# Kernel optimization log

Hardware: AMD Instinct MI355X
Metric: run time of the kernel (lower is better)

The kernel has to match this reference:

```python
import jax, jax.numpy as jnp
from jax import lax
import numpy as np

B, W, F, D = 48, 8192, 64, 128  # batch, input_window, c_in, d_model


def setup_inputs() -> dict:
    key = jax.random.key(0)
    k0, k1, k2, k3 = jax.random.split(key, 4)
    x = jax.random.normal(k0, (B, W, F), jnp.float32)
    # ContextConv(c_in->c_in, k=3): conv1d over time, zero 'same' padding (repo layer, assumed standard conv)
    ctx_w = jax.random.normal(k1, (F, F, 3), jnp.float32) * (2.0 / (F * 3)) ** 0.5
    ctx_b = jnp.zeros((F,), jnp.float32)
    # tokenConv: Conv1d(c_in -> d_model, k=3, circular padding, no bias), kaiming fan_in
    token_w = jax.random.normal(k2, (D, F, 3), jnp.float32) * (2.0 / (F * 3)) ** 0.5
    # seW: Linear(c_in -> input_window)
    seW_w = jax.random.normal(k3, (W, F), jnp.float32) * (1.0 / F) ** 0.5
    seW_b = jnp.zeros((W,), jnp.float32)
    return dict(x=x, ctx_w=ctx_w, ctx_b=ctx_b, token_w=token_w, seW_w=seW_w, seW_b=seW_b)


def _conv1d_ncw(x_ncw, w_oiw, padding):
    return lax.conv_general_dilated(
        x_ncw, w_oiw, window_strides=(1,), padding=padding,
        dimension_numbers=("NCW", "OIW", "NCW"))


def reference(x, ctx_w, ctx_b, token_w, seW_w, seW_b):
    # ---- contextConv: (B,W,F) -> (B,W,F), conv over time ----
    xc = _conv1d_ncw(x.transpose(0, 2, 1), ctx_w, [(1, 1)])  # (B,F,W)
    xc = (xc + ctx_b[None, :, None]).transpose(0, 2, 1)       # (B,W,F)

    # ---- structure_embedding (src is detached in torch) ----
    src = lax.stop_gradient(x)
    srcn = src / jnp.linalg.norm(src, axis=-1, keepdims=True)         # row-normalize each timestep
    gram = jnp.einsum('bwf,bwg->bfg', srcn, srcn)                      # batched f x f matmul
    xse = jax.nn.relu(jnp.einsum('bfg,wg->bfw', gram, seW_w) + seW_b[None, None, :])  # (B,F,W)
    xse = xse.transpose(0, 2, 1)                                       # (B,W,F)

    # ---- tokenConv with circular padding ----
    h = (xc + xse).transpose(0, 2, 1)                                  # (B,F,W)
    hp = jnp.pad(h, ((0, 0), (0, 0), (1, 1)), mode='wrap')
    out = _conv1d_ncw(hp, token_w, 'VALID')                            # (B,D,W)
    return out.transpose(0, 2, 1)                                      # (B,W,D)
```

## Files before the change

### kernel.cpp

```cpp
#include <hip/hip_runtime.h>
#include <stdint.h>

#define Bb 48
#define Ww 8192
#define Ff 64
#define Dd 128
#define TWt 64
#define NSLAB 32

#define WS_GRAMP 0u
#define WS_GRAM  25165824u
#define WS_TWT   25952256u
#define WS_CWT   26001408u
#define WS_GBF   26025984u
#define WS_SWB   26419200u
#define WS_RINV  27467776u
#define WS_XBF   29040640u
#define WS_TOTAL (29040640ull + 50331648ull)

typedef __bf16 bf16x8 __attribute__((ext_vector_type(8)));
typedef float f32x4 __attribute__((ext_vector_type(4)));

__device__ __forceinline__ float bf2f(unsigned short u){
  union { unsigned int i; float f; } v; v.i = ((unsigned int)u) << 16; return v.f;
}
__device__ __forceinline__ unsigned short f2bf(float f){
  union { float f; unsigned int i; } v; v.f = f;
  unsigned int i = v.i;
  return (unsigned short)((i + 0x7fffu + ((i >> 16) & 1u)) >> 16);
}
__device__ __forceinline__ f32x4 mfma16(bf16x8 a, bf16x8 b, f32x4 c){
  return __builtin_amdgcn_mfma_f32_16x16x32_bf16(a, b, c, 0, 0, 0);
}

__global__ __launch_bounds__(256) void pack_weights(const float* __restrict__ ctx_w,
                                                    const float* __restrict__ token_w,
                                                    unsigned short* __restrict__ cwT,
                                                    unsigned short* __restrict__ twT)
{
  int idx = blockIdx.x * 256 + threadIdx.x;
  const int ntw = Dd * 192;
  if (idx < ntw){
    int d = idx / 192, kim = idx % 192;
    int ktap = kim >> 6, fi = kim & 63;
    twT[idx] = f2bf(token_w[(d * Ff + fi) * 3 + ktap]);
  } else if (idx < ntw + Ff * 192){
    int i2 = idx - ntw;
    int f = i2 / 192, kim = i2 % 192;
    int ktap = kim >> 6, fi = kim & 63;
    cwT[i2] = f2bf(ctx_w[(f * Ff + fi) * 3 + ktap]);
  }
}

__global__ __launch_bounds__(256) void convert_sew(const float* __restrict__ src,
                                                   unsigned short* __restrict__ dst)
{
  int i = (blockIdx.x * 256 + threadIdx.x) * 8;
  float4 a0 = *(const float4*)(src + i);
  float4 a1 = *(const float4*)(src + i + 4);
  union { uint4 q; unsigned short s[8]; } u;
  u.s[0]=f2bf(a0.x); u.s[1]=f2bf(a0.y); u.s[2]=f2bf(a0.z); u.s[3]=f2bf(a0.w);
  u.s[4]=f2bf(a1.x); u.s[5]=f2bf(a1.y); u.s[6]=f2bf(a1.z); u.s[7]=f2bf(a1.w);
  *(uint4*)(dst + i) = u.q;
}

__global__ __launch_bounds__(256) void xprep(const float* __restrict__ x,
                                             unsigned short* __restrict__ xbf,
                                             float* __restrict__ rinvb)
{
  int tid = blockIdx.x * 256 + threadIdx.x;
  int row = tid >> 2;
  int f0  = (tid & 3) * 16;
  const float* xr = x + (size_t)row * Ff + f0;
  float v[16];
  *(float4*)(v)      = *(const float4*)(xr);
  *(float4*)(v + 4)  = *(const float4*)(xr + 4);
  *(float4*)(v + 8)  = *(const float4*)(xr + 8);
  *(float4*)(v + 12) = *(const float4*)(xr + 12);
  float ss = 0.f;
#pragma unroll
  for (int i = 0; i < 16; ++i) ss += v[i] * v[i];
  ss += __shfl_xor(ss, 1);
  ss += __shfl_xor(ss, 2);
  float rinv = rsqrtf(ss);
  union { uint4 q[2]; unsigned short s[16]; } u;
#pragma unroll
  for (int i = 0; i < 16; ++i) u.s[i] = f2bf(v[i]);
  unsigned short* dst = xbf + (size_t)row * Ff + f0;
  *(uint4*)(dst)     = u.q[0];
  *(uint4*)(dst + 8) = u.q[1];
  if ((tid & 3) == 0) rinvb[row] = rinv;
}

__global__ __launch_bounds__(256) void gram_kernel(const float* __restrict__ x,
                                                   const unsigned short* __restrict__ xbf,
                                                   const float* __restrict__ rinvb,
                                                   float* __restrict__ gramP,
                                                   int fast)
{
  const int b = blockIdx.y;
  const int w_base = blockIdx.x * (Ww / NSLAB);
  const int t = threadIdx.x;
  const int lane = t & 63;
  const int wave = t >> 6;
  const int lrow = lane & 15;
  const int lk = lane >> 4;

  __shared__ unsigned short st[64 * 72];

  f32x4 acc[4] = {};

  const int wl = t >> 2;
  const int f0 = (t & 3) * 16;

  for (int sc = 0; sc < (Ww / NSLAB) / 64; ++sc) {
    const int w0 = w_base + sc * 64;
    const size_t rowg = (size_t)b * Ww + (size_t)(w0 + wl);
    if (fast){
      union { uint4 q; unsigned short s[8]; } a0, a1;
      a0.q = *(const uint4*)(xbf + rowg * Ff + f0);
      a1.q = *(const uint4*)(xbf + rowg * Ff + f0 + 8);
      float rinv = rinvb[rowg];
#pragma unroll
      for (int i = 0; i < 8; ++i) st[(f0 + i) * 72 + wl]     = f2bf(bf2f(a0.s[i]) * rinv);
#pragma unroll
      for (int i = 0; i < 8; ++i) st[(f0 + 8 + i) * 72 + wl] = f2bf(bf2f(a1.s[i]) * rinv);
    } else {
      const float* xr = x + rowg * Ff + f0;
      float v[16];
      *(float4*)(v)      = *(const float4*)(xr);
      *(float4*)(v + 4)  = *(const float4*)(xr + 4);
      *(float4*)(v + 8)  = *(const float4*)(xr + 8);
      *(float4*)(v + 12) = *(const float4*)(xr + 12);
      float ss = 0.f;
#pragma unroll
      for (int i = 0; i < 16; ++i) ss += v[i] * v[i];
      ss += __shfl_xor(ss, 1);
      ss += __shfl_xor(ss, 2);
      float rinv = rsqrtf(ss);
#pragma unroll
      for (int i = 0; i < 16; ++i) st[(f0 + i) * 72 + wl] = f2bf(v[i] * rinv);
    }
    __syncthreads();
#pragma unroll
    for (int kc = 0; kc < 2; ++kc){
      const int kw = kc * 32 + lk * 8;
      bf16x8 bf = *(const bf16x8*)(st + (wave * 16 + lrow) * 72 + kw);
#pragma unroll
      for (int mt = 0; mt < 4; ++mt){
        bf16x8 af = *(const bf16x8*)(st + (mt * 16 + lrow) * 72 + kw);
        acc[mt] = mfma16(af, bf, acc[mt]);
      }
    }
    __syncthreads();
  }

  float* gb = gramP + ((size_t)(blockIdx.x * Bb + b)) * 4096;
#pragma unroll
  for (int mt = 0; mt < 4; ++mt)
#pragma unroll
    for (int r = 0; r < 4; ++r){
      int f = mt * 16 + lk * 4 + r;
      int g = wave * 16 + lrow;
      gb[f * 64 + g] = acc[mt][r];
    }
}

__global__ __launch_bounds__(256) void gram_reduce(const float* __restrict__ gramP,
                                                   float* __restrict__ gram,
                                                   unsigned short* __restrict__ gbf,
                                                   int fast)
{
  int i = blockIdx.x * 256 + threadIdx.x;
  int b = i >> 10;
  int q = i & 1023;
  float sx = 0.f, sy = 0.f, sz = 0.f, sw = 0.f;
#pragma unroll
  for (int sl = 0; sl < NSLAB; ++sl){
    const float4 v = *(const float4*)(gramP + (((size_t)(sl * Bb + b)) << 12) + q * 4);
    sx += v.x; sy += v.y; sz += v.z; sw += v.w;
  }
  float4 s = make_float4(sx, sy, sz, sw);
  *(float4*)(gram + (((size_t)b) << 12) + q * 4) = s;
  if (fast){
    union { unsigned long long u; unsigned short h[4]; } u;
    u.h[0] = f2bf(sx); u.h[1] = f2bf(sy); u.h[2] = f2bf(sz); u.h[3] = f2bf(sw);
    *(unsigned long long*)(gbf + (((size_t)b) << 12) + q * 4) = u.u;
  }
}

#define XSP 72
#define SSP 72
#define HSP 72

__global__ __launch_bounds__(256, 4) void fused_kernel(
    const float* __restrict__ x,
    const unsigned short* __restrict__ xbf,
    const float* __restrict__ ctx_b,
    const float* __restrict__ seW_w,
    const unsigned short* __restrict__ sWb,
    const float* __restrict__ seW_b,
    const float* __restrict__ gram,
    const unsigned short* __restrict__ gbf,
    const unsigned short* __restrict__ cwT,
    const unsigned short* __restrict__ twT,
    float* __restrict__ out,
    int fast)
{
  const int b = blockIdx.y;
  const int w0 = blockIdx.x * TWt;
  const int t = threadIdx.x;
  const int lane = t & 63;
  const int wave = t >> 6;
  const int lrow = lane & 15;
  const int lk = lane >> 4;

  __shared__ __align__(16) unsigned char smem[(84 * XSP + 80 * SSP + 66 * HSP) * 2];
  unsigned short* xs  = (unsigned short*)smem;
  unsigned short* sws = xs + 84 * XSP;
  unsigned short* hsh = sws + 80 * SSP;

  if (fast){
    for (int item = t; item < 84 * 8; item += 256){
      int i = item >> 3, seg = item & 7;
      int c = w0 - 2 + i;
      uint4 val = make_uint4(0u,0u,0u,0u);
      if (c >= 0 && c < Ww) val = *(const uint4*)(xbf + ((size_t)b*Ww + c)*Ff + seg*8);
      *(uint4*)(xs + i*XSP + seg*8) = val;
    }
    for (int item = t; item < 80 * 8; item += 256){
      int i = item >> 3, seg = item & 7;
      int hc = (w0 - 1 + i) & (Ww - 1);
      *(uint4*)(sws + i*SSP + seg*8) = *(const uint4*)(sWb + (size_t)hc*Ff + seg*8);
    }
  } else {
    for (int item = t; item < 84 * 8; item += 256){
      int i = item >> 3, seg = item & 7;
      int c = w0 - 2 + i;
      union { uint4 q; unsigned short s[8]; } u;
      if (c >= 0 && c < Ww){
        const float* xr = x + ((size_t)b*Ww + c)*Ff + seg*8;
        float4 a0 = *(const float4*)(xr);
        float4 a1 = *(const float4*)(xr + 4);
        u.s[0]=f2bf(a0.x); u.s[1]=f2bf(a0.y); u.s[2]=f2bf(a0.z); u.s[3]=f2bf(a0.w);
        u.s[4]=f2bf(a1.x); u.s[5]=f2bf(a1.y); u.s[6]=f2bf(a1.z); u.s[7]=f2bf(a1.w);
      } else {
        u.q = make_uint4(0u,0u,0u,0u);
      }
      *(uint4*)(xs + i*XSP + seg*8) = u.q;
    }
  }
  __syncthreads();

  const int nt = wave;
  bf16x8 cw_frag[6];
  {
    const unsigned short* p = cwT + (nt*16 + lrow)*192 + lk*8;
#pragma unroll
    for (int kc = 0; kc < 6; ++kc) cw_frag[kc] = *(const bf16x8*)(p + kc*32);
  }
  bf16x8 se_frag[2];
  if (fast){
    const unsigned short* gp = gbf + (size_t)b*4096 + (nt*16 + lrow)*64;
#pragma unroll
    for (int kc = 0; kc < 2; ++kc) se_frag[kc] = *(const bf16x8*)(gp + kc*32 + lk*8);
  } else {
    const float* gb = gram + (size_t)b * 4096;
#pragma unroll
    for (int kc = 0; kc < 2; ++kc){
      union { bf16x8 v; unsigned short s[8]; } u;
#pragma unroll
      for (int j = 0; j < 8; ++j){
        int g = kc*32 + lk*8 + j;
        u.s[j] = f2bf(gb[g*64 + nt*16 + lrow]);
      }
      se_frag[kc] = u.v;
    }
  }

  f32x4 xc_acc[5] = {};
  f32x4 se_acc[5] = {};

#pragma unroll
  for (int mt = 0; mt < 5; ++mt){
#pragma unroll
    for (int kc = 0; kc < 6; ++kc){
      int kim = kc*32 + lk*8;
      int ktap = kim >> 6, fi = kim & 63;
      bf16x8 a = *(const bf16x8*)(xs + (mt*16 + lrow + ktap)*XSP + fi);
      xc_acc[mt] = mfma16(a, cw_frag[kc], xc_acc[mt]);
    }
    if (fast){
#pragma unroll
      for (int kc = 0; kc < 2; ++kc){
        bf16x8 a = *(const bf16x8*)(sws + (mt*16 + lrow)*SSP + kc*32 + lk*8);
        se_acc[mt] = mfma16(a, se_frag[kc], se_acc[mt]);
      }
    } else {
      int hc = (w0 - 1 + mt*16 + lrow) & (Ww - 1);
      const float* sp = seW_w + (size_t)hc * Ff;
#pragma unroll
      for (int kc = 0; kc < 2; ++kc){
        union { bf16x8 v; unsigned short s[8]; } u;
        float4 a0 = *(const float4*)(sp + kc*32 + lk*8);
        float4 a1 = *(const float4*)(sp + kc*32 + lk*8 + 4);
        u.s[0]=f2bf(a0.x); u.s[1]=f2bf(a0.y); u.s[2]=f2bf(a0.z); u.s[3]=f2bf(a0.w);
        u.s[4]=f2bf(a1.x); u.s[5]=f2bf(a1.y); u.s[6]=f2bf(a1.z); u.s[7]=f2bf(a1.w);
        se_acc[mt] = mfma16(u.v, se_frag[kc], se_acc[mt]);
      }
    }
  }

  {
    float cb = ctx_b[nt*16 + lrow];
#pragma unroll
    for (int mt = 0; mt < 5; ++mt){
#pragma unroll
      for (int r = 0; r < 4; ++r){
        int j = mt*16 + lk*4 + r;
        if (j < 66){
          int hc = (w0 - 1 + j) & (Ww - 1);
          float se = se_acc[mt][r] + seW_b[hc];
          se = se > 0.f ? se : 0.f;
          hsh[j*HSP + nt*16 + lrow] = f2bf(xc_acc[mt][r] + cb + se);
        }
      }
    }
  }
  __syncthreads();

  if (blockIdx.x == 0 || blockIdx.x == (Ww/TWt - 1)){
    const int j  = (blockIdx.x == 0) ? 0 : 65;
    const int hc = (blockIdx.x == 0) ? (Ww - 1) : 0;
    if (t < 64){
      const int f = t;
      float a = ctx_b[f];
      for (int ktap = 0; ktap < 3; ++ktap){
        int c = hc + ktap - 1;
        if (c >= 0 && c < Ww){
          const float* xr = x + ((size_t)b*Ww + c)*Ff;
          const unsigned short* wr = cwT + f*192 + ktap*64;
          for (int fi = 0; fi < 64; ++fi) a += xr[fi] * bf2f(wr[fi]);
        }
      }
      const float* gb = gram + (size_t)b * 4096;
      const float* sp = seW_w + (size_t)hc * Ff;
      float se = seW_b[hc];
      for (int g = 0; g < 64; ++g) se += sp[g] * gb[g*64 + f];
      se = se > 0.f ? se : 0.f;
      hsh[j*HSP + f] = f2bf(a + se);
    }
    __syncthreads();
  }

  bf16x8 tw_frag[2][6];
#pragma unroll
  for (int q = 0; q < 2; ++q){
    const unsigned short* p = twT + ((wave*2 + q)*16 + lrow)*192 + lk*8;
#pragma unroll
    for (int kc = 0; kc < 6; ++kc) tw_frag[q][kc] = *(const bf16x8*)(p + kc*32);
  }
  f32x4 oacc[4][2] = {};
#pragma unroll
  for (int mt = 0; mt < 4; ++mt){
#pragma unroll
    for (int kc = 0; kc < 6; ++kc){
      int kim = kc*32 + lk*8;
      int ktap = kim >> 6, fi = kim & 63;
      bf16x8 a = *(const bf16x8*)(hsh + (mt*16 + lrow + ktap)*HSP + fi);
#pragma unroll
      for (int q = 0; q < 2; ++q)
        oacc[mt][q] = mfma16(a, tw_frag[q][kc], oacc[mt][q]);
    }
  }

#pragma unroll
  for (int mt = 0; mt < 4; ++mt){
#pragma unroll
    for (int q = 0; q < 2; ++q)
#pragma unroll
      for (int r = 0; r < 4; ++r){
        int row = w0 + mt*16 + lk*4 + r;
        int d   = (wave*2 + q)*16 + lrow;
        out[((size_t)b*Ww + row)*Dd + d] = oacc[mt][q][r];
      }
  }
}

extern "C" void kernel_launch(void* const* d_in, const int* in_sizes, int n_in,
                              void* d_out, int out_size, void* d_ws, size_t ws_size,
                              hipStream_t stream)
{
  const float* x       = (const float*)d_in[0];
  const float* ctx_w   = (const float*)d_in[1];
  const float* ctx_b   = (const float*)d_in[2];
  const float* token_w = (const float*)d_in[3];
  const float* seW_w   = (const float*)d_in[4];
  const float* seW_b   = (const float*)d_in[5];
  float* out = (float*)d_out;

  char* ws = (char*)d_ws;
  float*          gramP = (float*)(ws + WS_GRAMP);
  float*          gram  = (float*)(ws + WS_GRAM);
  unsigned short* twT   = (unsigned short*)(ws + WS_TWT);
  unsigned short* cwT   = (unsigned short*)(ws + WS_CWT);
  unsigned short* gbf   = (unsigned short*)(ws + WS_GBF);
  unsigned short* sWb   = (unsigned short*)(ws + WS_SWB);
  float*          rinvb = (float*)(ws + WS_RINV);
  unsigned short* xbf   = (unsigned short*)(ws + WS_XBF);

  const int fast = (ws_size >= (size_t)WS_TOTAL) ? 1 : 0;

  pack_weights<<<dim3(144), dim3(256), 0, stream>>>(ctx_w, token_w, cwT, twT);
  if (fast){
    convert_sew<<<dim3(256), dim3(256), 0, stream>>>(seW_w, sWb);
    xprep<<<dim3(6144), dim3(256), 0, stream>>>(x, xbf, rinvb);
  }
  gram_kernel<<<dim3(NSLAB, Bb), dim3(256), 0, stream>>>(x, xbf, rinvb, gramP, fast);
  gram_reduce<<<dim3(192), dim3(256), 0, stream>>>(gramP, gram, gbf, fast);
  fused_kernel<<<dim3(Ww/TWt, Bb), dim3(256), 0, stream>>>(
      x, xbf, ctx_b, seW_w, sWb, seW_b, gram, gbf, cwT, twT, out, fast);
}
```

Baseline: 370.8 us.

## Fuse x bf16 conversion into gram kernel, merge weight prep, alias LDS

After: 382.0 us. +3.0%, slower.

```diff
diff --git a/kernel.cpp b/kernel.cpp
--- a/kernel.cpp
+++ b/kernel.cpp
@@ -14,9 +14,8 @@
 #define WS_CWT   26001408u
 #define WS_GBF   26025984u
 #define WS_SWB   26419200u
-#define WS_RINV  27467776u
-#define WS_XBF   29040640u
-#define WS_TOTAL (29040640ull + 50331648ull)
+#define WS_XBF   27467776u
+#define WS_TOTAL (27467776ull + 50331648ull)
 
 typedef __bf16 bf16x8 __attribute__((ext_vector_type(8)));
 typedef float f32x4 __attribute__((ext_vector_type(4)));
@@ -33,70 +32,43 @@
   return __builtin_amdgcn_mfma_f32_16x16x32_bf16(a, b, c, 0, 0, 0);
 }
 
-__global__ __launch_bounds__(256) void pack_weights(const float* __restrict__ ctx_w,
+__global__ __launch_bounds__(256) void prep_weights(const float* __restrict__ ctx_w,
                                                     const float* __restrict__ token_w,
+                                                    const float* __restrict__ seW_w,
                                                     unsigned short* __restrict__ cwT,
-                                                    unsigned short* __restrict__ twT)
+                                                    unsigned short* __restrict__ twT,
+                                                    unsigned short* __restrict__ sWb,
+                                                    int fast)
 {
-  int idx = blockIdx.x * 256 + threadIdx.x;
-  const int ntw = Dd * 192;
-  if (idx < ntw){
-    int d = idx / 192, kim = idx % 192;
-    int ktap = kim >> 6, fi = kim & 63;
-    twT[idx] = f2bf(token_w[(d * Ff + fi) * 3 + ktap]);
-  } else if (idx < ntw + Ff * 192){
-    int i2 = idx - ntw;
-    int f = i2 / 192, kim = i2 % 192;
-    int ktap = kim >> 6, fi = kim & 63;
-    cwT[i2] = f2bf(ctx_w[(f * Ff + fi) * 3 + ktap]);
-  }
-}
-
-__global__ __launch_bounds__(256) void convert_sew(const float* __restrict__ src,
-                                                   unsigned short* __restrict__ dst)
-{
-  int i = (blockIdx.x * 256 + threadIdx.x) * 8;
-  float4 a0 = *(const float4*)(src + i);
-  float4 a1 = *(const float4*)(src + i + 4);
-  union { uint4 q; unsigned short s[8]; } u;
-  u.s[0]=f2bf(a0.x); u.s[1]=f2bf(a0.y); u.s[2]=f2bf(a0.z); u.s[3]=f2bf(a0.w);
-  u.s[4]=f2bf(a1.x); u.s[5]=f2bf(a1.y); u.s[6]=f2bf(a1.z); u.s[7]=f2bf(a1.w);
-  *(uint4*)(dst + i) = u.q;
-}
-
-__global__ __launch_bounds__(256) void xprep(const float* __restrict__ x,
-                                             unsigned short* __restrict__ xbf,
-                                             float* __restrict__ rinvb)
-{
-  int tid = blockIdx.x * 256 + threadIdx.x;
-  int row = tid >> 2;
-  int f0  = (tid & 3) * 16;
-  const float* xr = x + (size_t)row * Ff + f0;
-  float v[16];
-  *(float4*)(v)      = *(const float4*)(xr);
-  *(float4*)(v + 4)  = *(const float4*)(xr + 4);
-  *(float4*)(v + 8)  = *(const float4*)(xr + 8);
-  *(float4*)(v + 12) = *(const float4*)(xr + 12);
-  float ss = 0.f;
-#pragma unroll
-  for (int i = 0; i < 16; ++i) ss += v[i] * v[i];
-  ss += __shfl_xor(ss, 1);
-  ss += __shfl_xor(ss, 2);
-  float rinv = rsqrtf(ss);
-  union { uint4 q[2]; unsigned short s[16]; } u;
-#pragma unroll
-  for (int i = 0; i < 16; ++i) u.s[i] = f2bf(v[i]);
-  unsigned short* dst = xbf + (size_t)row * Ff + f0;
-  *(uint4*)(dst)     = u.q[0];
-  *(uint4*)(dst + 8) = u.q[1];
-  if ((tid & 3) == 0) rinvb[row] = rinv;
+  const int bx = blockIdx.x;
+  if (bx < 144){
+    int idx = bx * 256 + threadIdx.x;
+    const int ntw = Dd * 192;
+    if (idx < ntw){
+      int d = idx / 192, kim = idx % 192;
+      int ktap = kim >> 6, fi = kim & 63;
+      twT[idx] = f2bf(token_w[(d * Ff + fi) * 3 + ktap]);
+    } else if (idx < ntw + Ff * 192){
+      int i2 = idx - ntw;
+      int f = i2 / 192, kim = i2 % 192;
+      int ktap = kim >> 6, fi = kim & 63;
+      cwT[i2] = f2bf(ctx_w[(f * Ff + fi) * 3 + ktap]);
+    }
+  } else if (fast){
+    int i = ((bx - 144) * 256 + threadIdx.x) * 8;
+    float4 a0 = *(const float4*)(seW_w + i);
+    float4 a1 = *(const float4*)(seW_w + i + 4);
+    union { uint4 q; unsigned short s[8]; } u;
+    u.s[0]=f2bf(a0.x); u.s[1]=f2bf(a0.y); u.s[2]=f2bf(a0.z); u.s[3]=f2bf(a0.w);
+    u.s[4]=f2bf(a1.x); u.s[5]=f2bf(a1.y); u.s[6]=f2bf(a1.z); u.s[7]=f2bf(a1.w);
+    *(uint4*)(sWb + i) = u.q;
+  }
 }
 
 __global__ __launch_bounds__(256) void gram_kernel(const float* __restrict__ x,
-                                                   const unsigned short* __restrict__ xbf,
-                                                   const float* __restrict__ rinvb,
+                                                   unsigned short* __restrict__ xbf,
                                                    float* __restrict__ gramP,
-                                                   int fast)
+                                                   int writeXbf)
 {
   const int b = blockIdx.y;
   const int w_base = blockIdx.x * (Ww / NSLAB);
@@ -113,46 +85,63 @@
   const int wl = t >> 2;
   const int f0 = (t & 3) * 16;
 
-  for (int sc = 0; sc < (Ww / NSLAB) / 64; ++sc) {
-    const int w0 = w_base + sc * 64;
-    const size_t rowg = (size_t)b * Ww + (size_t)(w0 + wl);
-    if (fast){
-      union { uint4 q; unsigned short s[8]; } a0, a1;
-      a0.q = *(const uint4*)(xbf + rowg * Ff + f0);
-      a1.q = *(const uint4*)(xbf + rowg * Ff + f0 + 8);
-      float rinv = rinvb[rowg];
-#pragma unroll
-      for (int i = 0; i < 8; ++i) st[(f0 + i) * 72 + wl]     = f2bf(bf2f(a0.s[i]) * rinv);
-#pragma unroll
-      for (int i = 0; i < 8; ++i) st[(f0 + 8 + i) * 72 + wl] = f2bf(bf2f(a1.s[i]) * rinv);
-    } else {
-      const float* xr = x + rowg * Ff + f0;
-      float v[16];
-      *(float4*)(v)      = *(const float4*)(xr);
-      *(float4*)(v + 4)  = *(const float4*)(xr + 4);
-      *(float4*)(v + 8)  = *(const float4*)(xr + 8);
-      *(float4*)(v + 12) = *(const float4*)(xr + 12);
-      float ss = 0.f;
-#pragma unroll
-      for (int i = 0; i < 16; ++i) ss += v[i] * v[i];
-      ss += __shfl_xor(ss, 1);
-      ss += __shfl_xor(ss, 2);
-      float rinv = rsqrtf(ss);
-#pragma unroll
-      for (int i = 0; i < 16; ++i) st[(f0 + i) * 72 + wl] = f2bf(v[i] * rinv);
-    }
+  float v[16];
+  {
+    const float* xr = x + ((size_t)b * Ww + (size_t)(w_base + wl)) * Ff + f0;
+    *(float4*)(v)      = *(const float4*)(xr);
+    *(float4*)(v + 4)  = *(const float4*)(xr + 4);
+    *(float4*)(v + 8)  = *(const float4*)(xr + 8);
+    *(float4*)(v + 12) = *(const float4*)(xr + 12);
+  }
+
+  for (int sc = 0; sc < 4; ++sc) {
+    const size_t rowg = (size_t)b * Ww + (size_t)(w_base + sc * 64 + wl);
+
+    float ss = 0.f;
+#pragma unroll
+    for (int i = 0; i < 16; ++i) ss += v[i] * v[i];
+    ss += __shfl_xor(ss, 1);
+    ss += __shfl_xor(ss, 2);
+    float rinv = rsqrtf(ss);
+
+    union { uint4 q[2]; unsigned short s[16]; } u;
+#pragma unroll
+    for (int i = 0; i < 16; ++i){
+      u.s[i] = f2bf(v[i]);
+      st[(f0 + i) * 72 + wl] = f2bf(v[i] * rinv);
+    }
+    if (writeXbf){
+      unsigned short* dst = xbf + rowg * Ff + f0;
+      *(uint4*)(dst)     = u.q[0];
+      *(uint4*)(dst + 8) = u.q[1];
+    }
+
+    float vn[16];
+    if (sc < 3){
+      const float* xr = x + ((size_t)b * Ww + (size_t)(w_base + (sc+1) * 64 + wl)) * Ff + f0;
+      *(float4*)(vn)      = *(const float4*)(xr);
+      *(float4*)(vn + 4)  = *(const float4*)(xr + 4);
+      *(float4*)(vn + 8)  = *(const float4*)(xr + 8);
+      *(float4*)(vn + 12) = *(const float4*)(xr + 12);
+    }
+
     __syncthreads();
 #pragma unroll
     for (int kc = 0; kc < 2; ++kc){
       const int kw = kc * 32 + lk * 8;
-      bf16x8 bf = *(const bf16x8*)(st + (wave * 16 + lrow) * 72 + kw);
+      bf16x8 bfr = *(const bf16x8*)(st + (wave * 16 + lrow) * 72 + kw);
 #pragma unroll
       for (int mt = 0; mt < 4; ++mt){
         bf16x8 af = *(const bf16x8*)(st + (mt * 16 + lrow) * 72 + kw);
-        acc[mt] = mfma16(af, bf, acc[mt]);
+        acc[mt] = mfma16(af, bfr, acc[mt]);
       }
     }
     __syncthreads();
+
+    if (sc < 3){
+#pragma unroll
+      for (int i = 0; i < 16; ++i) v[i] = vn[i];
+    }
   }
 
   float* gb = gramP + ((size_t)(blockIdx.x * Bb + b)) * 4096;
@@ -193,7 +182,7 @@
 #define SSP 72
 #define HSP 72
 
-__global__ __launch_bounds__(256, 4) void fused_kernel(
+__global__ __launch_bounds__(256, 6) void fused_kernel(
     const float* __restrict__ x,
     const unsigned short* __restrict__ xbf,
     const float* __restrict__ ctx_b,
@@ -215,10 +204,10 @@
   const int lrow = lane & 15;
   const int lk = lane >> 4;
 
-  __shared__ __align__(16) unsigned char smem[(84 * XSP + 80 * SSP + 66 * HSP) * 2];
+  __shared__ __align__(16) unsigned char smem[(84 * XSP + 80 * SSP) * 2];
   unsigned short* xs  = (unsigned short*)smem;
   unsigned short* sws = xs + 84 * XSP;
-  unsigned short* hsh = sws + 80 * SSP;
+  unsigned short* hsh = xs;
 
   if (fast){
     for (int item = t; item < 84 * 8; item += 256){
@@ -311,6 +300,8 @@
     }
   }
 
+  __syncthreads();
+
   {
     float cb = ctx_b[nt*16 + lrow];
 #pragma unroll
@@ -406,17 +397,12 @@
   unsigned short* cwT   = (unsigned short*)(ws + WS_CWT);
   unsigned short* gbf   = (unsigned short*)(ws + WS_GBF);
   unsigned short* sWb   = (unsigned short*)(ws + WS_SWB);
-  float*          rinvb = (float*)(ws + WS_RINV);
   unsigned short* xbf   = (unsigned short*)(ws + WS_XBF);
 
   const int fast = (ws_size >= (size_t)WS_TOTAL) ? 1 : 0;
 
-  pack_weights<<<dim3(144), dim3(256), 0, stream>>>(ctx_w, token_w, cwT, twT);
-  if (fast){
-    convert_sew<<<dim3(256), dim3(256), 0, stream>>>(seW_w, sWb);
-    xprep<<<dim3(6144), dim3(256), 0, stream>>>(x, xbf, rinvb);
-  }
-  gram_kernel<<<dim3(NSLAB, Bb), dim3(256), 0, stream>>>(x, xbf, rinvb, gramP, fast);
+  prep_weights<<<dim3(400), dim3(256), 0, stream>>>(ctx_w, token_w, seW_w, cwT, twT, sWb, fast);
+  gram_kernel<<<dim3(NSLAB, Bb), dim3(256), 0, stream>>>(x, xbf, gramP, fast);
   gram_reduce<<<dim3(192), dim3(256), 0, stream>>>(gramP, gram, gbf, fast);
   fused_kernel<<<dim3(Ww/TWt, Bb), dim3(256), 0, stream>>>(
       x, xbf, ctx_b, seW_w, sWb, seW_b, gram, gbf, cwT, twT, out, fast);
```
